# Kernel tuning notes

Measured on AMD Instinct MI355X. Metric: run time of the kernel, lower is better.

The kernel has to match this reference:

```python
import jax, jax.numpy as jnp
import numpy as np
import math

B, N, T, C, H = 8, 1024, 512, 1024, 16
D = C // H

def _ln(x, g, b, eps=1e-5):
    m = jnp.mean(x, axis=-1, keepdims=True)
    v = jnp.var(x, axis=-1, keepdims=True)
    return (x - m) * jax.lax.rsqrt(v + eps) * g + b

def _heads(x, L):
    return x.reshape(B, L, H, D).transpose(0, 2, 1, 3)  # [B,H,L,D]

def setup_inputs() -> dict:
    key = jax.random.key(0)
    ks = jax.random.split(key, 12)
    s = 0.02
    return {
        "prev_output": jax.random.normal(ks[0], (B, N, C), jnp.float32),
        "encoder_output": jax.random.normal(ks[1], (B, T, C), jnp.float32),
        "sa_w": jax.random.normal(ks[2], (C, 3 * C), jnp.float32) * s,
        "sa_b": jnp.zeros((3 * C,), jnp.float32),
        "sa_pw": jax.random.normal(ks[3], (C, C), jnp.float32) * s,
        "sa_pb": jnp.zeros((C,), jnp.float32),
        "caq_w": jax.random.normal(ks[4], (C, C), jnp.float32) * s,
        "caq_b": jnp.zeros((C,), jnp.float32),
        "cakv_w": jax.random.normal(ks[5], (C, 2 * C), jnp.float32) * s,
        "cakv_b": jnp.zeros((2 * C,), jnp.float32),
        "ca_pw": jax.random.normal(ks[6], (C, C), jnp.float32) * s,
        "ca_pb": jnp.zeros((C,), jnp.float32),
        "fc_w": jax.random.normal(ks[7], (C, 4 * C), jnp.float32) * s,
        "fc_b": jnp.zeros((4 * C,), jnp.float32),
        "proj_w": jax.random.normal(ks[8], (4 * C, C), jnp.float32) * s,
        "proj_b": jnp.zeros((C,), jnp.float32),
        "ln1_g": jnp.ones((C,), jnp.float32), "ln1_b": jnp.zeros((C,), jnp.float32),
        "ln2_g": jnp.ones((C,), jnp.float32), "ln2_b": jnp.zeros((C,), jnp.float32),
        "ln3_g": jnp.ones((C,), jnp.float32), "ln3_b": jnp.zeros((C,), jnp.float32),
    }

def reference(prev_output, encoder_output, sa_w, sa_b, sa_pw, sa_pb,
              caq_w, caq_b, cakv_w, cakv_b, ca_pw, ca_pb,
              fc_w, fc_b, proj_w, proj_b,
              ln1_g, ln1_b, ln2_g, ln2_b, ln3_g, ln3_b):
    scale = 1.0 / math.sqrt(D)
    # --- masked self-attention (note: no residual in original code) ---
    qkv = prev_output @ sa_w + sa_b  # [B,N,3C]
    q, k, v = jnp.split(qkv, 3, axis=-1)
    q, k, v = _heads(q, N), _heads(k, N), _heads(v, N)
    att = jnp.einsum('bhnd,bhmd->bhnm', q, k) * scale
    causal = jnp.tril(jnp.ones((N, N), bool))
    att = jnp.where(causal, att, -jnp.inf)
    att = jax.nn.softmax(att, axis=-1)
    y = jnp.einsum('bhnm,bhmd->bhnd', att, v).transpose(0, 2, 1, 3).reshape(B, N, C)
    x = y @ sa_pw + sa_pb
    x = _ln(x, ln1_g, ln1_b)
    # --- cross-attention with residual ---
    kv = encoder_output @ cakv_w + cakv_b  # [B,T,2C]
    k2, v2 = jnp.split(kv, 2, axis=-1)
    q2 = _heads(x @ caq_w + caq_b, N)
    k2, v2 = _heads(k2, T), _heads(v2, T)
    att2 = jax.nn.softmax(jnp.einsum('bhnd,bhtd->bhnt', q2, k2) * scale, axis=-1)
    y2 = jnp.einsum('bhnt,bhtd->bhnd', att2, v2).transpose(0, 2, 1, 3).reshape(B, N, C)
    x = x + (y2 @ ca_pw + ca_pb)
    x = _ln(x, ln2_g, ln2_b)
    # --- MLP with residual ---
    h = jax.nn.gelu(x @ fc_w + fc_b, approximate=False)
    x = x + (h @ proj_w + proj_b)
    return _ln(x, ln3_g, ln3_b)
```

## Files before the change

kernel.cpp:

```cpp
#include <hip/hip_runtime.h>

typedef unsigned short u16;
typedef unsigned int u32;
typedef __attribute__((ext_vector_type(8))) short short8;
typedef __attribute__((ext_vector_type(4))) float f32x4;
typedef __attribute__((ext_vector_type(16))) float f32x16;

__device__ __forceinline__ u16 f2bf(float f) {
  union { float f; unsigned int u; } v; v.f = f;
  unsigned int r = v.u + 0x7FFFu + ((v.u >> 16) & 1u);
  return (u16)(r >> 16);
}
__device__ __forceinline__ float bf2f(u16 b) {
  union { unsigned int u; float f; } v; v.u = ((unsigned int)b) << 16;
  return v.f;
}

__device__ __forceinline__ void gload_lds16(const void* g, void* l) {
  __builtin_amdgcn_global_load_lds((const __attribute__((address_space(1))) void*)g,
                                   (__attribute__((address_space(3))) void*)l, 16, 0, 0);
}

__device__ __forceinline__ u32 cvtpk_bf16(float lo, float hi) {
  u32 r;
  asm("v_cvt_pk_bf16_f32 %0, %1, %2" : "=v"(r) : "v"(lo), "v"(hi));
  return r;
}

__device__ __forceinline__ void plswap32(u32& a, u32& b) {
#if __has_builtin(__builtin_amdgcn_permlane32_swap)
  auto r = __builtin_amdgcn_permlane32_swap((int)a, (int)b, false, false);
  a = (u32)r[0]; b = (u32)r[1];
#else
  asm volatile("v_permlane32_swap_b32 %0, %1" : "+v"(a), "+v"(b));
#endif
}

__device__ __forceinline__ void plswapf(float& a, float& b) {
  union { float f; u32 u; } x, y; x.f = a; y.f = b;
  plswap32(x.u, y.u);
  a = x.f; b = y.f;
}

template <int N>
__device__ __forceinline__ void wait_vm() {
  if constexpr (N == 0) asm volatile("s_waitcnt vmcnt(0)" ::: "memory");
  else if constexpr (N == 3) asm volatile("s_waitcnt vmcnt(3)" ::: "memory");
  else if constexpr (N == 4) asm volatile("s_waitcnt vmcnt(4)" ::: "memory");
  else if constexpr (N == 6) asm volatile("s_waitcnt vmcnt(6)" ::: "memory");
  else if constexpr (N == 8) asm volatile("s_waitcnt vmcnt(8)" ::: "memory");
}
__device__ __forceinline__ void wait_lgkm0() {
  asm volatile("s_waitcnt lgkmcnt(0)" ::: "memory");
}
__device__ __forceinline__ void lgkm_gate(int n) {
  switch (n) {
    case 0: asm volatile("s_waitcnt lgkmcnt(0)" ::: "memory"); break;
    case 1: asm volatile("s_waitcnt lgkmcnt(1)" ::: "memory"); break;
    case 2: asm volatile("s_waitcnt lgkmcnt(2)" ::: "memory"); break;
    case 3: asm volatile("s_waitcnt lgkmcnt(3)" ::: "memory"); break;
    case 4: asm volatile("s_waitcnt lgkmcnt(4)" ::: "memory"); break;
    case 5: asm volatile("s_waitcnt lgkmcnt(5)" ::: "memory"); break;
    case 6: asm volatile("s_waitcnt lgkmcnt(6)" ::: "memory"); break;
    default: asm volatile("s_waitcnt lgkmcnt(7)" ::: "memory"); break;
  }
}
#define SBAR() __builtin_amdgcn_sched_barrier(0)

__device__ __forceinline__ u32 lds_off(const void* p) {
  return (u32)(size_t)(const __attribute__((address_space(3))) void*)p;
}
__device__ __forceinline__ short8 ds_read128(u32 off) {
  short8 d;
  asm volatile("ds_read_b128 %0, %1" : "=v"(d) : "v"(off));
  return d;
}

__global__ __launch_bounds__(256) void cvt_f32_bf16(const float* __restrict__ in,
                                                    u16* __restrict__ out, long n) {
  long i = ((long)blockIdx.x * 256 + threadIdx.x) * 4;
  if (i + 3 < n) {
    float4 v = *(const float4*)(in + i);
    unsigned long long p = (unsigned long long)f2bf(v.x) |
                           ((unsigned long long)f2bf(v.y) << 16) |
                           ((unsigned long long)f2bf(v.z) << 32) |
                           ((unsigned long long)f2bf(v.w) << 48);
    *(unsigned long long*)(out + i) = p;
  }
}

__global__ __launch_bounds__(256) void wtrans(const float* __restrict__ W,
                                              u16* __restrict__ WT, int K, int N) {
  __shared__ float t[32][33];
  int n0 = blockIdx.x * 32, k0 = blockIdx.y * 32;
  int tx = threadIdx.x, ty = threadIdx.y;
#pragma unroll
  for (int r = 0; r < 4; r++)
    t[ty + r * 8][tx] = W[(long)(k0 + ty + r * 8) * N + n0 + tx];
  __syncthreads();
#pragma unroll
  for (int r = 0; r < 4; r++)
    WT[(long)(n0 + ty + r * 8) * K + k0 + tx] = f2bf(t[tx][ty + r * 8]);
}

__global__ __launch_bounds__(256) void vtrans(const u16* __restrict__ src,
                                              u16* __restrict__ dst,
                                              int rows, int rstride, int head_off, int H) {
  __shared__ u16 t[64][65];
  int bh = blockIdx.y;
  int b = bh / H, h = bh % H;
  long n0 = (long)blockIdx.x * 64;
  const u16* s = src + (long)b * rows * rstride + head_off + h * 64;
  int q = threadIdx.x >> 6, ln = threadIdx.x & 63;
#pragma unroll
  for (int r = 0; r < 16; r++) {
    int nl = q * 16 + r;
    t[nl][ln] = s[(n0 + nl) * (long)rstride + ln];
  }
  __syncthreads();
  u16* d = dst + (long)bh * 64 * rows;
#pragma unroll
  for (int r = 0; r < 16; r++) {
    int dd = q * 16 + r;
    d[(long)dd * rows + n0 + ln] = t[ln][dd];
  }
}

template <int BN, int WM, int GELU>
__global__ __launch_bounds__(512, 1) void gemm4(const u16* __restrict__ A,
                                                const u16* __restrict__ BT,
                                                const float* __restrict__ bias,
                                                float* __restrict__ outF,
                                                u16* __restrict__ outB,
                                                int M, int N, int K) {
  constexpr int BM = 256;
  constexpr int WN = 8 / WM;
  constexpr int MR = BM / (16 * WM);
  constexpr int NR = BN / (16 * WN);
  constexpr int BLB = BN / 128;
  constexpr int LH = 2 + BLB;
  __shared__ __align__(16) u16 Al[2][2][BM * 32];
  __shared__ __align__(16) u16 Bl[2][2][BN * 32];
  const int tid = threadIdx.x;
  const int w = tid >> 6, l = tid & 63;
  const int wr = w / WN, wc = w % WN;
  const int lr = l & 15, lg = l >> 4;

  const int nx = M >> 8;
  const int gpx = nx >> 3;
  const int hgt = blockIdx.x;
  const int xcd = hgt & 7, j = hgt >> 3;
  const int bx = xcd * gpx + (j % gpx);
  const int by = j / gpx;
  const long m0 = (long)bx * BM, n0 = (long)by * BN;

  const int nt = K >> 6;

  const u16* baseA[2];
#pragma unroll
  for (int rr = 0; rr < 2; rr++) {
    int e = rr * 512 + tid, row = e >> 2;
    int kk = ((e & 3) - (row >> 1)) & 3;
    baseA[rr] = A + (m0 + row) * (long)K + kk * 8;
  }
  const u16* baseB[BLB];
#pragma unroll
  for (int rr = 0; rr < BLB; rr++) {
    int e = rr * 512 + tid, row = e >> 2;
    int kk = ((e & 3) - (row >> 1)) & 3;
    baseB[rr] = BT + (n0 + row) * (long)K + kk * 8;
  }

  auto stage = [&](int buf, int kh, int t) {
    if (t < nt) {
#pragma unroll
      for (int rr = 0; rr < 2; rr++)
        gload_lds16(baseA[rr] + (long)t * 64 + kh * 32, &Al[buf][kh][(rr * 512 + tid) * 8]);
#pragma unroll
      for (int rr = 0; rr < BLB; rr++)
        gload_lds16(baseB[rr] + (long)t * 64 + kh * 32, &Bl[buf][kh][(rr * 512 + tid) * 8]);
    }
  };

  f32x4 acc[MR][NR];
#pragma unroll
  for (int i = 0; i < MR; i++)
#pragma unroll
    for (int nn = 0; nn < NR; nn++) acc[i][nn] = (f32x4){0.f, 0.f, 0.f, 0.f};

  stage(0, 0, 0); stage(0, 1, 0); stage(1, 0, 1);
  wait_vm<2 * LH>();
  SBAR(); __builtin_amdgcn_s_barrier(); SBAR();

  for (int t = 0; t < nt; ++t) {
    const int bt = t & 1, nb = bt ^ 1;
#pragma unroll
    for (int kh = 0; kh < 2; kh++) {
      const u16* Ah = &Al[bt][kh][0];
      const u16* Bh = &Bl[bt][kh][0];
      short8 bf[NR], af[MR];
#pragma unroll
      for (int nn = 0; nn < NR; nn++) {
        int row = wc * (BN / WN) + nn * 16 + lr;
        bf[nn] = ds_read128(lds_off(&Bh[row * 32 + (((lg + (row >> 1)) & 3) << 3)]));
      }
#pragma unroll
      for (int mm = 0; mm < MR; mm++) {
        int row = wr * (BM / WM) + mm * 16 + lr;
        af[mm] = ds_read128(lds_off(&Ah[row * 32 + (((lg + (row >> 1)) & 3) << 3)]));
      }
      if (kh == 0) stage(nb, 1, t + 1); else stage(bt, 0, t + 2);
      __builtin_amdgcn_s_setprio(1);
#pragma unroll
      for (int mm = 0; mm < MR; mm++) {
        lgkm_gate(MR - 1 - mm);
        SBAR();
#pragma unroll
        for (int nn = 0; nn < NR; nn++)
          acc[mm][nn] = __builtin_amdgcn_mfma_f32_16x16x32_bf16(af[mm], bf[nn], acc[mm][nn], 0, 0, 0);
      }
      __builtin_amdgcn_s_setprio(0);
      if (kh == 0) {
        if (t == nt - 1) wait_vm<0>(); else wait_vm<2 * LH>();
      } else {
        if (t + 2 < nt) wait_vm<2 * LH>();
        else if (t + 1 < nt) wait_vm<LH>();
      }
      SBAR(); __builtin_amdgcn_s_barrier(); SBAR();
    }
  }

  float bv[NR];
#pragma unroll
  for (int nn = 0; nn < NR; nn++)
    bv[nn] = bias ? bias[n0 + wc * (BN / WN) + nn * 16 + lr] : 0.f;
#pragma unroll
  for (int mm = 0; mm < MR; mm++) {
#pragma unroll
    for (int i = 0; i < 4; i++) {
      const long row = m0 + wr * (BM / WM) + mm * 16 + lg * 4 + i;
#pragma unroll
      for (int nn = 0; nn < NR; nn++) {
        const long col = n0 + wc * (BN / WN) + nn * 16 + lr;
        float v = acc[mm][nn][i] + bv[nn];
        if (GELU) v = 0.5f * v * (1.f + erff(v * 0.70710678118654752f));
        if (outF) outF[row * N + col] = v;
        if (outB) outB[row * N + col] = f2bf(v);
      }
    }
  }
}

template <bool CAUSAL>
__global__ __launch_bounds__(256, 4) void attn3(const u16* __restrict__ qb, long q_bstride, int q_rstride,
                                                const u16* __restrict__ kbp, long k_bstride, int k_rstride,
                                                const u16* __restrict__ vt,
                                                u16* __restrict__ yb, long y_bstride, int y_rstride,
                                                int Nk, int H) {
  __shared__ __align__(16) u16 Kl[2][2048];
  __shared__ __align__(16) u16 Vl[2][2048];
  const int tid = threadIdx.x;
  const int w = tid >> 6, l = tid & 63;
  const int qi = l & 31, hi = l >> 5;

  const int nwg = gridDim.x;
  const int chunk = nwg >> 3;
  const int nb = (blockIdx.x & 7) * chunk + (blockIdx.x >> 3);
  const int bh = nb >> 3;
  const int bx6 = nb & 7;
  const int bx = (bx6 & 1) ? (7 - (bx6 >> 1)) : (bx6 >> 1);
  const int b = bh / H, h = bh % H;
  const int qr0 = bx * 128 + w * 32;
  const u16* qp = qb + (long)b * q_bstride + h * 64;
  const u16* kp = kbp + (long)b * k_bstride + h * 64;
  const u16* vp = vt + (long)bh * 64 * Nk;
  const float CL = 0.125f * 1.44269504088896340736f;

  const u16* qrow = qp + (long)(qr0 + qi) * q_rstride + hi * 8;
  short8 qf0 = *(const short8*)(qrow);
  short8 qf1 = *(const short8*)(qrow + 16);
  short8 qf2 = *(const short8*)(qrow + 32);
  short8 qf3 = *(const short8*)(qrow + 48);

  f32x16 ot0, ot1;
#pragma unroll
  for (int i = 0; i < 16; i++) { ot0[i] = 0.f; ot1[i] = 0.f; }
  float m_run = -INFINITY, l_run = 0.f;

  const int krow_ = tid >> 3, kcb_ = (tid & 7) ^ (krow_ & 7);
  const int vrow_ = tid >> 2, vcb_ = (tid & 3) ^ (vrow_ & 3);
  const u16* kg = kp + (long)krow_ * k_rstride + kcb_ * 8;
  const u16* vg = vp + (long)vrow_ * Nk + vcb_ * 8;

  const int ntiles = CAUSAL ? (bx * 4 + 4) : (Nk >> 5);
  const int mytile = bx * 4 + w;

  gload_lds16(kg, &Kl[0][tid * 8]);
  gload_lds16(vg, &Vl[0][tid * 8]);
  __syncthreads();

  for (int t = 0; t < ntiles; ++t) {
    const int cur = t & 1;
    if (t + 1 < ntiles) {
      gload_lds16(kg + (t + 1) * 32 * (long)k_rstride, &Kl[cur ^ 1][tid * 8]);
      gload_lds16(vg + (t + 1) * 32, &Vl[cur ^ 1][tid * 8]);
    }
    if (!CAUSAL || t <= mytile) {
      const int kb0 = t * 32;
      const bool dmask = CAUSAL && (t == mytile);
      short8 kf[4];
#pragma unroll
      for (int ks = 0; ks < 4; ks++)
        kf[ks] = *(const short8*)&Kl[cur][(qi << 6) + (((2 * ks + hi) ^ (qi & 7)) << 3)];
      f32x16 sc;
#pragma unroll
      for (int i = 0; i < 16; i++) sc[i] = 0.f;
      sc = __builtin_amdgcn_mfma_f32_32x32x16_bf16(kf[0], qf0, sc, 0, 0, 0);
      sc = __builtin_amdgcn_mfma_f32_32x32x16_bf16(kf[1], qf1, sc, 0, 0, 0);
      sc = __builtin_amdgcn_mfma_f32_32x32x16_bf16(kf[2], qf2, sc, 0, 0, 0);
      sc = __builtin_amdgcn_mfma_f32_32x32x16_bf16(kf[3], qf3, sc, 0, 0, 0);
      if (dmask) {
#pragma unroll
        for (int r = 0; r < 16; r++) {
          int key = kb0 + (r & 3) + 8 * (r >> 2) + 4 * hi;
          if (key > qr0 + qi) sc[r] = -INFINITY;
        }
      }
      float mx = sc[0];
#pragma unroll
      for (int r = 1; r < 16; r++) mx = fmaxf(mx, sc[r]);
      { float a = mx, bb2 = mx; plswapf(a, bb2); mx = fmaxf(a, bb2); }
      float mnew = fmaxf(m_run, mx);
      float alpha = exp2f((m_run - mnew) * CL);
      m_run = mnew;
      float p[16];
      float ssum = 0.f;
#pragma unroll
      for (int r = 0; r < 16; r++) { p[r] = exp2f((sc[r] - mnew) * CL); ssum += p[r]; }
      { float a = ssum, bb2 = ssum; plswapf(a, bb2); ssum = a + bb2; }
      l_run = l_run * alpha + ssum;
#pragma unroll
      for (int i = 0; i < 16; i++) { ot0[i] *= alpha; ot1[i] *= alpha; }
      u32 w0 = cvtpk_bf16(p[0], p[1]);
      u32 w1 = cvtpk_bf16(p[2], p[3]);
      u32 w2 = cvtpk_bf16(p[4], p[5]);
      u32 w3 = cvtpk_bf16(p[6], p[7]);
      plswap32(w0, w2);
      plswap32(w1, w3);
      u32 w4 = cvtpk_bf16(p[8], p[9]);
      u32 w5 = cvtpk_bf16(p[10], p[11]);
      u32 w6 = cvtpk_bf16(p[12], p[13]);
      u32 w7 = cvtpk_bf16(p[14], p[15]);
      plswap32(w4, w6);
      plswap32(w5, w7);
      union { u32 u[4]; short8 s; } ua0, ua1;
      ua0.u[0] = w0; ua0.u[1] = w1; ua0.u[2] = w2; ua0.u[3] = w3;
      ua1.u[0] = w4; ua1.u[1] = w5; ua1.u[2] = w6; ua1.u[3] = w7;
      short8 va00 = *(const short8*)&Vl[cur][(qi << 5) + (((hi) ^ (qi & 3)) << 3)];
      short8 va01 = *(const short8*)&Vl[cur][(qi << 5) + (((2 + hi) ^ (qi & 3)) << 3)];
      short8 va10 = *(const short8*)&Vl[cur][((qi + 32) << 5) + (((hi) ^ (qi & 3)) << 3)];
      short8 va11 = *(const short8*)&Vl[cur][((qi + 32) << 5) + (((2 + hi) ^ (qi & 3)) << 3)];
      ot0 = __builtin_amdgcn_mfma_f32_32x32x16_bf16(va00, ua0.s, ot0, 0, 0, 0);
      ot0 = __builtin_amdgcn_mfma_f32_32x32x16_bf16(va01, ua1.s, ot0, 0, 0, 0);
      ot1 = __builtin_amdgcn_mfma_f32_32x32x16_bf16(va10, ua0.s, ot1, 0, 0, 0);
      ot1 = __builtin_amdgcn_mfma_f32_32x32x16_bf16(va11, ua1.s, ot1, 0, 0, 0);
    }
    __syncthreads();
  }

  float inv = 1.f / l_run;
  u16* yp = yb + (long)b * y_bstride + h * 64 + (long)(qr0 + qi) * y_rstride;
#pragma unroll
  for (int g = 0; g < 4; g++) {
    uint2 s0;
    s0.x = cvtpk_bf16(ot0[4 * g + 0] * inv, ot0[4 * g + 1] * inv);
    s0.y = cvtpk_bf16(ot0[4 * g + 2] * inv, ot0[4 * g + 3] * inv);
    *(uint2*)(yp + 8 * g + 4 * hi) = s0;
    uint2 s1;
    s1.x = cvtpk_bf16(ot1[4 * g + 0] * inv, ot1[4 * g + 1] * inv);
    s1.y = cvtpk_bf16(ot1[4 * g + 2] * inv, ot1[4 * g + 3] * inv);
    *(uint2*)(yp + 32 + 8 * g + 4 * hi) = s1;
  }
}

template <int BFIN>
__global__ __launch_bounds__(256) void ln2_k(const void* __restrict__ xv,
                                             const float* __restrict__ res,
                                             const float* __restrict__ g,
                                             const float* __restrict__ bb,
                                             float* __restrict__ outF,
                                             u16* __restrict__ outB, int C) {
  __shared__ float red[8];
  long row = blockIdx.x;
  int i0 = threadIdx.x * 4;
  float x0, x1, x2, x3;
  if (BFIN) {
    const u16* xp = (const u16*)xv + row * C + i0;
    unsigned long long pk = *(const unsigned long long*)xp;
    x0 = bf2f((u16)(pk));
    x1 = bf2f((u16)(pk >> 16));
    x2 = bf2f((u16)(pk >> 32));
    x3 = bf2f((u16)(pk >> 48));
  } else {
    float4 v = *(const float4*)((const float*)xv + row * C + i0);
    x0 = v.x; x1 = v.y; x2 = v.z; x3 = v.w;
  }
  if (res) {
    float4 r = *(const float4*)(res + row * C + i0);
    x0 += r.x; x1 += r.y; x2 += r.z; x3 += r.w;
  }
  float s = x0 + x1 + x2 + x3;
  float sq = x0 * x0 + x1 * x1 + x2 * x2 + x3 * x3;
#pragma unroll
  for (int off = 1; off < 64; off <<= 1) {
    s += __shfl_xor(s, off, 64);
    sq += __shfl_xor(sq, off, 64);
  }
  int w = threadIdx.x >> 6, l = threadIdx.x & 63;
  if (l == 0) { red[w] = s; red[4 + w] = sq; }
  __syncthreads();
  s = red[0] + red[1] + red[2] + red[3];
  sq = red[4] + red[5] + red[6] + red[7];
  float mean = s * (1.f / 1024.f);
  float var = sq * (1.f / 1024.f) - mean * mean;
  float rstd = rsqrtf(var + 1e-5f);
  float4 gv = *(const float4*)(g + i0);
  float4 bv = *(const float4*)(bb + i0);
  float o0 = (x0 - mean) * rstd * gv.x + bv.x;
  float o1 = (x1 - mean) * rstd * gv.y + bv.y;
  float o2 = (x2 - mean) * rstd * gv.z + bv.z;
  float o3 = (x3 - mean) * rstd * gv.w + bv.w;
  if (outF) {
    float4 ov; ov.x = o0; ov.y = o1; ov.z = o2; ov.w = o3;
    *(float4*)(outF + row * C + i0) = ov;
  }
  if (outB) {
    unsigned long long p = (unsigned long long)f2bf(o0) |
                           ((unsigned long long)f2bf(o1) << 16) |
                           ((unsigned long long)f2bf(o2) << 32) |
                           ((unsigned long long)f2bf(o3) << 48);
    *(unsigned long long*)(outB + row * C + i0) = p;
  }
}

template <int BFIN>
__global__ __launch_bounds__(256) void ln2r_k(const void* __restrict__ xv,
                                              const float* __restrict__ res,
                                              const float* __restrict__ g,
                                              const float* __restrict__ bb,
                                              float* __restrict__ resOut,
                                              float* __restrict__ outF,
                                              u16* __restrict__ outB, int C) {
  __shared__ float red[8];
  long row = blockIdx.x;
  int i0 = threadIdx.x * 4;
  float x0, x1, x2, x3;
  if (BFIN) {
    const u16* xp = (const u16*)xv + row * C + i0;
    unsigned long long pk = *(const unsigned long long*)xp;
    x0 = bf2f((u16)(pk));
    x1 = bf2f((u16)(pk >> 16));
    x2 = bf2f((u16)(pk >> 32));
    x3 = bf2f((u16)(pk >> 48));
  } else {
    float4 v = *(const float4*)((const float*)xv + row * C + i0);
    x0 = v.x; x1 = v.y; x2 = v.z; x3 = v.w;
  }
  if (res) {
    float4 r = *(const float4*)(res + row * C + i0);
    x0 += r.x; x1 += r.y; x2 += r.z; x3 += r.w;
  }
  if (resOut) {
    float4 ov; ov.x = x0; ov.y = x1; ov.z = x2; ov.w = x3;
    *(float4*)(resOut + row * C + i0) = ov;
  }
  float s = x0 + x1 + x2 + x3;
  float sq = x0 * x0 + x1 * x1 + x2 * x2 + x3 * x3;
#pragma unroll
  for (int off = 1; off < 64; off <<= 1) {
    s += __shfl_xor(s, off, 64);
    sq += __shfl_xor(sq, off, 64);
  }
  int w = threadIdx.x >> 6, l = threadIdx.x & 63;
  if (l == 0) { red[w] = s; red[4 + w] = sq; }
  __syncthreads();
  s = red[0] + red[1] + red[2] + red[3];
  sq = red[4] + red[5] + red[6] + red[7];
  float mean = s * (1.f / 1024.f);
  float var = sq * (1.f / 1024.f) - mean * mean;
  float rstd = rsqrtf(var + 1e-5f);
  float4 gv = *(const float4*)(g + i0);
  float4 bv = *(const float4*)(bb + i0);
  float o0 = (x0 - mean) * rstd * gv.x + bv.x;
  float o1 = (x1 - mean) * rstd * gv.y + bv.y;
  float o2 = (x2 - mean) * rstd * gv.z + bv.z;
  float o3 = (x3 - mean) * rstd * gv.w + bv.w;
  if (outF) {
    float4 ov; ov.x = o0; ov.y = o1; ov.z = o2; ov.w = o3;
    *(float4*)(outF + row * C + i0) = ov;
  }
  if (outB) {
    unsigned long long p = (unsigned long long)f2bf(o0) |
                           ((unsigned long long)f2bf(o1) << 16) |
                           ((unsigned long long)f2bf(o2) << 32) |
                           ((unsigned long long)f2bf(o3) << 48);
    *(unsigned long long*)(outB + row * C + i0) = p;
  }
}

extern "C" void kernel_launch(void* const* d_in, const int* in_sizes, int n_in,
                              void* d_out, int out_size, void* d_ws, size_t ws_size,
                              hipStream_t stream) {
  const int B = 8, N = 1024, T = 512, C = 1024, H = 16;
  const float* prev = (const float*)d_in[0];
  const float* enc = (const float*)d_in[1];
  const float* sa_w = (const float*)d_in[2];
  const float* sa_b = (const float*)d_in[3];
  const float* sa_pw = (const float*)d_in[4];
  const float* sa_pb = (const float*)d_in[5];
  const float* caq_w = (const float*)d_in[6];
  const float* caq_b = (const float*)d_in[7];
  const float* cakv_w = (const float*)d_in[8];
  const float* cakv_b = (const float*)d_in[9];
  const float* ca_pw = (const float*)d_in[10];
  const float* ca_pb = (const float*)d_in[11];
  const float* fc_w = (const float*)d_in[12];
  const float* fc_b = (const float*)d_in[13];
  const float* proj_w = (const float*)d_in[14];
  const float* proj_b = (const float*)d_in[15];
  const float* ln1_g = (const float*)d_in[16];
  const float* ln1_b = (const float*)d_in[17];
  const float* ln2_g = (const float*)d_in[18];
  const float* ln2_b = (const float*)d_in[19];
  const float* ln3_g = (const float*)d_in[20];
  const float* ln3_b = (const float*)d_in[21];

  char* ws = (char*)d_ws;
  u16* wT_sa   = (u16*)(ws + 0);
  u16* wT_sapw = (u16*)(ws + 6291456);
  u16* wT_caq  = (u16*)(ws + 8388608);
  u16* wT_cakv = (u16*)(ws + 10485760);
  u16* wT_capw = (u16*)(ws + 14680064);
  u16* wT_fc   = (u16*)(ws + 16777216);
  u16* wT_proj = (u16*)(ws + 25165824);
  u16* abf   = (u16*)(ws + 33554432);
  u16* encbf = (u16*)(ws + 50331648);
  u16* qkv   = (u16*)(ws + 58720256);
  u16* vt1   = (u16*)(ws + 109051904);
  u16* ybf   = (u16*)(ws + 125829120);
  u16* pbf   = (u16*)(ws + 142606336);
  float* x1f  = (float*)(ws + 176160768);
  u16* x1bf  = (u16*)(ws + 209715200);
  u16* kvbf  = (u16*)(ws + 226492416);
  u16* y2bf  = abf;
  u16* vt2   = encbf;
  u16* q2bf  = ybf;
  u16* hbf   = qkv;

  cvt_f32_bf16<<<8192, 256, 0, stream>>>(prev, abf, (long)B * N * C);
  cvt_f32_bf16<<<4096, 256, 0, stream>>>(enc, encbf, (long)B * T * C);
  wtrans<<<dim3(96, 32), dim3(32, 8), 0, stream>>>(sa_w, wT_sa, 1024, 3072);
  wtrans<<<dim3(32, 32), dim3(32, 8), 0, stream>>>(sa_pw, wT_sapw, 1024, 1024);
  wtrans<<<dim3(32, 32), dim3(32, 8), 0, stream>>>(caq_w, wT_caq, 1024, 1024);
  wtrans<<<dim3(64, 32), dim3(32, 8), 0, stream>>>(cakv_w, wT_cakv, 1024, 2048);
  wtrans<<<dim3(32, 32), dim3(32, 8), 0, stream>>>(ca_pw, wT_capw, 1024, 1024);
  wtrans<<<dim3(128, 32), dim3(32, 8), 0, stream>>>(fc_w, wT_fc, 1024, 4096);
  wtrans<<<dim3(32, 128), dim3(32, 8), 0, stream>>>(proj_w, wT_proj, 4096, 1024);
  gemm4<128, 4, 0><<<768, 512, 0, stream>>>(abf, wT_sa, sa_b, nullptr, qkv, 8192, 3072, 1024);
  vtrans<<<dim3(16, 128), 256, 0, stream>>>(qkv, vt1, 1024, 3 * C, 2 * C, H);
  attn3<true><<<dim3(1024), 256, 0, stream>>>(qkv, (long)N * 3 * C, 3 * C,
                                              qkv + C, (long)N * 3 * C, 3 * C,
                                              vt1, ybf, (long)N * C, C, N, H);
  gemm4<128, 4, 0><<<256, 512, 0, stream>>>(ybf, wT_sapw, sa_pb, nullptr, pbf, 8192, 1024, 1024);
  ln2_k<1><<<8192, 256, 0, stream>>>(pbf, nullptr, ln1_g, ln1_b, x1f, x1bf, C);
  gemm4<128, 4, 0><<<256, 512, 0, stream>>>(x1bf, wT_caq, caq_b, nullptr, q2bf, 8192, 1024, 1024);
  gemm4<128, 4, 0><<<256, 512, 0, stream>>>(encbf, wT_cakv, cakv_b, nullptr, kvbf, 4096, 2048, 1024);
  vtrans<<<dim3(8, 128), 256, 0, stream>>>(kvbf, vt2, 512, 2 * C, C, H);
  attn3<false><<<dim3(1024), 256, 0, stream>>>(q2bf, (long)N * C, C,
                                               kvbf, (long)T * 2 * C, 2 * C,
                                               vt2, y2bf, (long)N * C, C, T, H);
  gemm4<128, 4, 0><<<256, 512, 0, stream>>>(y2bf, wT_capw, ca_pb, nullptr, pbf, 8192, 1024, 1024);
  ln2r_k<1><<<8192, 256, 0, stream>>>(pbf, x1f, ln2_g, ln2_b, x1f, nullptr, x1bf, C);
  gemm4<256, 2, 1><<<512, 512, 0, stream>>>(x1bf, wT_fc, fc_b, nullptr, hbf, 8192, 4096, 1024);
  gemm4<128, 4, 0><<<256, 512, 0, stream>>>(hbf, wT_proj, proj_b, nullptr, pbf, 8192, 1024, 4096);
  ln2_k<1><<<8192, 256, 0, stream>>>(pbf, x1f, ln3_g, ln3_b, (float*)d_out, nullptr, C);
}
```

Measured before the change: 525.6 us.

## Add 128x128-tile 256-thread GEMM kernel for the N=1024 projection GEMMs

```diff
diff --git a/kernel.cpp b/kernel.cpp
--- a/kernel.cpp
+++ b/kernel.cpp
@@ -242,6 +242,121 @@
 #pragma unroll
       for (int nn = 0; nn < NR; nn++) {
         const long col = n0 + wc * (BN / WN) + nn * 16 + lr;
+        float v = acc[mm][nn][i] + bv[nn];
+        if (GELU) v = 0.5f * v * (1.f + erff(v * 0.70710678118654752f));
+        if (outF) outF[row * N + col] = v;
+        if (outB) outB[row * N + col] = f2bf(v);
+      }
+    }
+  }
+}
+
+template <int GELU>
+__global__ __launch_bounds__(256, 2) void gemm8(const u16* __restrict__ A,
+                                                const u16* __restrict__ BT,
+                                                const float* __restrict__ bias,
+                                                float* __restrict__ outF,
+                                                u16* __restrict__ outB,
+                                                int M, int N, int K) {
+  constexpr int LH = 4;
+  __shared__ __align__(16) u16 Al[2][2][128 * 32];
+  __shared__ __align__(16) u16 Bl[2][2][128 * 32];
+  const int tid = threadIdx.x;
+  const int w = tid >> 6, l = tid & 63;
+  const int wr = w >> 1, wc = w & 1;
+  const int lr = l & 15, lg = l >> 4;
+
+  const int nx = M >> 7;
+  const int gpx = nx >> 3;
+  const int hgt = blockIdx.x;
+  const int xcd = hgt & 7, j = hgt >> 3;
+  const int bx = xcd * gpx + (j % gpx);
+  const int by = j / gpx;
+  const long m0 = (long)bx * 128, n0 = (long)by * 128;
+
+  const int nt = K >> 6;
+
+  const u16* baseA[2];
+  const u16* baseB[2];
+#pragma unroll
+  for (int rr = 0; rr < 2; rr++) {
+    int e = rr * 256 + tid, row = e >> 2;
+    int kk = ((e & 3) - (row >> 1)) & 3;
+    baseA[rr] = A + (m0 + row) * (long)K + kk * 8;
+    baseB[rr] = BT + (n0 + row) * (long)K + kk * 8;
+  }
+
+  auto stage = [&](int buf, int kh, int t) {
+    if (t < nt) {
+#pragma unroll
+      for (int rr = 0; rr < 2; rr++)
+        gload_lds16(baseA[rr] + (long)t * 64 + kh * 32, &Al[buf][kh][(rr * 256 + tid) * 8]);
+#pragma unroll
+      for (int rr = 0; rr < 2; rr++)
+        gload_lds16(baseB[rr] + (long)t * 64 + kh * 32, &Bl[buf][kh][(rr * 256 + tid) * 8]);
+    }
+  };
+
+  f32x4 acc[4][4];
+#pragma unroll
+  for (int i = 0; i < 4; i++)
+#pragma unroll
+    for (int nn = 0; nn < 4; nn++) acc[i][nn] = (f32x4){0.f, 0.f, 0.f, 0.f};
+
+  stage(0, 0, 0); stage(0, 1, 0); stage(1, 0, 1);
+  wait_vm<2 * LH>();
+  SBAR(); __builtin_amdgcn_s_barrier(); SBAR();
+
+  for (int t = 0; t < nt; ++t) {
+    const int bt = t & 1, nb = bt ^ 1;
+#pragma unroll
+    for (int kh = 0; kh < 2; kh++) {
+      const u16* Ah = &Al[bt][kh][0];
+      const u16* Bh = &Bl[bt][kh][0];
+      short8 bf[4], af[4];
+#pragma unroll
+      for (int nn = 0; nn < 4; nn++) {
+        int row = wc * 64 + nn * 16 + lr;
+        bf[nn] = ds_read128(lds_off(&Bh[row * 32 + (((lg + (row >> 1)) & 3) << 3)]));
+      }
+#pragma unroll
+      for (int mm = 0; mm < 4; mm++) {
+        int row = wr * 64 + mm * 16 + lr;
+        af[mm] = ds_read128(lds_off(&Ah[row * 32 + (((lg + (row >> 1)) & 3) << 3)]));
+      }
+      if (kh == 0) stage(nb, 1, t + 1); else stage(bt, 0, t + 2);
+      __builtin_amdgcn_s_setprio(1);
+#pragma unroll
+      for (int mm = 0; mm < 4; mm++) {
+        lgkm_gate(3 - mm);
+        SBAR();
+#pragma unroll
+        for (int nn = 0; nn < 4; nn++)
+          acc[mm][nn] = __builtin_amdgcn_mfma_f32_16x16x32_bf16(af[mm], bf[nn], acc[mm][nn], 0, 0, 0);
+      }
+      __builtin_amdgcn_s_setprio(0);
+      if (kh == 0) {
+        if (t == nt - 1) wait_vm<0>(); else wait_vm<2 * LH>();
+      } else {
+        if (t + 2 < nt) wait_vm<2 * LH>();
+        else if (t + 1 < nt) wait_vm<LH>();
+      }
+      SBAR(); __builtin_amdgcn_s_barrier(); SBAR();
+    }
+  }
+
+  float bv[4];
+#pragma unroll
+  for (int nn = 0; nn < 4; nn++)
+    bv[nn] = bias ? bias[n0 + wc * 64 + nn * 16 + lr] : 0.f;
+#pragma unroll
+  for (int mm = 0; mm < 4; mm++) {
+#pragma unroll
+    for (int i = 0; i < 4; i++) {
+      const long row = m0 + wr * 64 + mm * 16 + lg * 4 + i;
+#pragma unroll
+      for (int nn = 0; nn < 4; nn++) {
+        const long col = n0 + wc * 64 + nn * 16 + lr;
         float v = acc[mm][nn][i] + bv[nn];
         if (GELU) v = 0.5f * v * (1.f + erff(v * 0.70710678118654752f));
         if (outF) outF[row * N + col] = v;
@@ -571,17 +686,17 @@
   attn3<true><<<dim3(1024), 256, 0, stream>>>(qkv, (long)N * 3 * C, 3 * C,
                                               qkv + C, (long)N * 3 * C, 3 * C,
                                               vt1, ybf, (long)N * C, C, N, H);
-  gemm4<128, 4, 0><<<256, 512, 0, stream>>>(ybf, wT_sapw, sa_pb, nullptr, pbf, 8192, 1024, 1024);
+  gemm8<0><<<512, 256, 0, stream>>>(ybf, wT_sapw, sa_pb, nullptr, pbf, 8192, 1024, 1024);
   ln2_k<1><<<8192, 256, 0, stream>>>(pbf, nullptr, ln1_g, ln1_b, x1f, x1bf, C);
-  gemm4<128, 4, 0><<<256, 512, 0, stream>>>(x1bf, wT_caq, caq_b, nullptr, q2bf, 8192, 1024, 1024);
-  gemm4<128, 4, 0><<<256, 512, 0, stream>>>(encbf, wT_cakv, cakv_b, nullptr, kvbf, 4096, 2048, 1024);
+  gemm8<0><<<512, 256, 0, stream>>>(x1bf, wT_caq, caq_b, nullptr, q2bf, 8192, 1024, 1024);
+  gemm8<0><<<512, 256, 0, stream>>>(encbf, wT_cakv, cakv_b, nullptr, kvbf, 4096, 2048, 1024);
   vtrans<<<dim3(8, 128), 256, 0, stream>>>(kvbf, vt2, 512, 2 * C, C, H);
   attn3<false><<<dim3(1024), 256, 0, stream>>>(q2bf, (long)N * C, C,
                                                kvbf, (long)T * 2 * C, 2 * C,
                                                vt2, y2bf, (long)N * C, C, T, H);
-  gemm4<128, 4, 0><<<256, 512, 0, stream>>>(y2bf, wT_capw, ca_pb, nullptr, pbf, 8192, 1024, 1024);
+  gemm8<0><<<512, 256, 0, stream>>>(y2bf, wT_capw, ca_pb, nullptr, pbf, 8192, 1024, 1024);
   ln2r_k<1><<<8192, 256, 0, stream>>>(pbf, x1f, ln2_g, ln2_b, x1f, nullptr, x1bf, C);
   gemm4<256, 2, 1><<<512, 512, 0, stream>>>(x1bf, wT_fc, fc_b, nullptr, hbf, 8192, 4096, 1024);
-  gemm4<128, 4, 0><<<256, 512, 0, stream>>>(hbf, wT_proj, proj_b, nullptr, pbf, 8192, 1024, 4096);
+  gemm8<0><<<512, 256, 0, stream>>>(hbf, wT_proj, proj_b, nullptr, pbf, 8192, 1024, 4096);
   ln2_k<1><<<8192, 256, 0, stream>>>(pbf, x1f, ln3_g, ln3_b, (float*)d_out, nullptr, C);
 }
```

Result: slower. 540.5 us (+2.8%).
